# Performance work log

Measured on AMD Instinct MI355X. Metric: run time of the kernel, lower is better.

Reference implementation:

```python
import jax, jax.numpy as jnp
import numpy as np

N_NODES = 100000
N_EDGES = 1600000
N_GRAPHS = 1000
D_IN = 128
HID = 128
OUT = 6


def setup_inputs() -> dict:
    key = jax.random.key(0)
    ks = jax.random.split(key, 12)
    s = 1.0 / np.sqrt(HID)
    x = jax.random.normal(ks[0], (N_NODES, D_IN), dtype=jnp.float32)
    ei = jax.random.randint(ks[1], (2, N_EDGES), 0, N_NODES, dtype=jnp.int64)
    batch = jnp.sort(jax.random.randint(ks[2], (N_NODES,), 0, N_GRAPHS, dtype=jnp.int64))
    return {
        "x": x,
        "ei": ei,
        "batch": batch,
        "W1a": jax.random.normal(ks[3], (D_IN, HID), dtype=jnp.float32) * s,
        "b1a": jnp.zeros((HID,), jnp.float32),
        "W1b": jax.random.normal(ks[4], (HID, HID), dtype=jnp.float32) * s,
        "b1b": jnp.zeros((HID,), jnp.float32),
        "W2a": jax.random.normal(ks[5], (HID, HID), dtype=jnp.float32) * s,
        "b2a": jnp.zeros((HID,), jnp.float32),
        "W2b": jax.random.normal(ks[6], (HID, HID), dtype=jnp.float32) * s,
        "b2b": jnp.zeros((HID,), jnp.float32),
        "Wlin": jax.random.normal(ks[7], (HID, OUT), dtype=jnp.float32) * s,
        "blin": jnp.zeros((OUT,), jnp.float32),
    }


def _gin_conv(x, src, dst, Wa, ba, Wb, bb):
    # PyG GINConv (eps=0): mlp(x_i + sum_{j->i} x_j)
    agg = jax.ops.segment_sum(x[src], dst, num_segments=N_NODES)
    h = agg + x
    h = jnp.maximum(h @ Wa + ba, 0.0)
    return h @ Wb + bb


def reference(x, ei, batch, W1a, b1a, W1b, b1b, W2a, b2a, W2b, b2b, Wlin, blin):
    src, dst = ei[0], ei[1]
    h = jnp.maximum(_gin_conv(x, src, dst, W1a, b1a, W1b, b1b), 0.0)
    # dropout is identity in eval mode
    h = _gin_conv(h, src, dst, W2a, b2a, W2b, b2b)
    # global mean pool per graph
    sums = jax.ops.segment_sum(h, batch, num_segments=N_GRAPHS)
    cnts = jax.ops.segment_sum(jnp.ones((h.shape[0], 1), h.dtype), batch, num_segments=N_GRAPHS)
    pooled = sums / jnp.maximum(cnts, 1.0)
    return pooled @ Wlin + blin
```

## Files before the change

kernel.cpp:

```cpp
#include <hip/hip_runtime.h>

#define N_NODES 100000
#define N_EDGES 1600000
#define N_GRAPHS 1000
#define HID 128
#define OUTD 6

#define BUCK_LOG 7
#define BUCK_W (1 << BUCK_LOG)
#define NBUCK ((N_NODES + BUCK_W - 1) >> BUCK_LOG)
#define BCAP 4096
#define FILL_BLOCKS 256
#define FILL_CHUNK ((N_EDGES + FILL_BLOCKS - 1) / FILL_BLOCKS)

#define CVT_BLOCKS 6250
#define GST_BLOCKS 391
#define PACK_BLOCKS 32
#define PREP_BLOCKS (CVT_BLOCKS + GST_BLOCKS + PACK_BLOCKS + FILL_BLOCKS)

typedef _Float16 h2 __attribute__((ext_vector_type(2)));
typedef _Float16 half8 __attribute__((ext_vector_type(8)));
typedef float f32x4 __attribute__((ext_vector_type(4)));

__global__ __launch_bounds__(256) void k_prep(const float* __restrict__ x,
                                              const int* __restrict__ batch,
                                              const int* __restrict__ srcv,
                                              const int* __restrict__ dstv,
                                              const float* __restrict__ W1a,
                                              const float* __restrict__ W1b,
                                              const float* __restrict__ W2a,
                                              const float* __restrict__ W2b,
                                              _Float16* __restrict__ X16,
                                              int* __restrict__ gstart,
                                              _Float16* __restrict__ P,
                                              int* __restrict__ bcur0,
                                              int* __restrict__ packed) {
    __shared__ int h[NBUCK];
    __shared__ int lcur[NBUCK];
    int b = blockIdx.x, t = threadIdx.x;
    if (b < CVT_BLOCKS) {
        size_t i = ((size_t)b * 256 + t) * 8;
        float4 v0 = *(const float4*)(x + i);
        float4 v1 = *(const float4*)(x + i + 4);
        half8 o;
        o[0] = (_Float16)v0.x; o[1] = (_Float16)v0.y; o[2] = (_Float16)v0.z; o[3] = (_Float16)v0.w;
        o[4] = (_Float16)v1.x; o[5] = (_Float16)v1.y; o[6] = (_Float16)v1.z; o[7] = (_Float16)v1.w;
        *(half8*)(X16 + i) = o;
    } else if (b < CVT_BLOCKS + GST_BLOCKS) {
        int n = (b - CVT_BLOCKS) * 256 + t;
        if (n < N_NODES) {
            int bb = batch[n];
            int prev = (n == 0) ? -1 : batch[n - 1];
            for (int g = prev + 1; g <= bb; ++g) gstart[g] = n;
            if (n == N_NODES - 1)
                for (int g = bb + 1; g <= N_GRAPHS; ++g) gstart[g] = N_NODES;
        }
    } else if (b < CVT_BLOCKS + GST_BLOCKS + PACK_BLOCKS) {
        int gid = (b - CVT_BLOCKS - GST_BLOCKS) * 256 + t;
        int mat = gid >> 11;
        int r = gid & 2047;
        int ctks = r >> 6;
        int lane = r & 63;
        int col = (ctks >> 2) * 16 + (lane & 15);
        int k0 = (ctks & 3) * 32 + (lane >> 4) * 8;
        const float* W = (mat == 0) ? W1a : (mat == 1) ? W1b : (mat == 2) ? W2a : W2b;
        _Float16* dp = P + mat * 16384 + r * 8;
#pragma unroll
        for (int j = 0; j < 8; ++j) dp[j] = (_Float16)W[(k0 + j) * HID + col];
    } else {
        int bb = b - (CVT_BLOCKS + GST_BLOCKS + PACK_BLOCKS);
        int e0 = bb * FILL_CHUNK;
        int e1 = min(e0 + FILL_CHUNK, N_EDGES);
        for (int i = t; i < NBUCK; i += 256) h[i] = 0;
        __syncthreads();
        for (int e = e0 + t; e < e1; e += 256) atomicAdd(&h[dstv[e] >> BUCK_LOG], 1);
        __syncthreads();
        for (int i = t; i < NBUCK; i += 256) {
            int c = h[i];
            lcur[i] = c ? atomicAdd(&bcur0[i], c) : 0;
        }
        __syncthreads();
        for (int e = e0 + t; e < e1; e += 256) {
            int d = dstv[e];
            int bk = d >> BUCK_LOG;
            int pos = atomicAdd(&lcur[bk], 1);
            if (pos < BCAP) packed[bk * BCAP + pos] = ((d & (BUCK_W - 1)) << 20) | srcv[e];
        }
    }
}

__global__ __launch_bounds__(256) void k_csrfine(const int* __restrict__ packed,
                                                 const int* __restrict__ bcur0,
                                                 int* __restrict__ offsets,
                                                 int* __restrict__ csr_src) {
    __shared__ int hist[BUCK_W];
    __shared__ int scan[BUCK_W];
    __shared__ int cur[BUCK_W];
    __shared__ int red[4];
    int b = blockIdx.x;
    int base = b << BUCK_LOG;
    int t = threadIdx.x;
    int partial = 0;
    for (int j = t; j < b; j += 256) partial += bcur0[j];
#pragma unroll
    for (int d = 32; d > 0; d >>= 1) partial += __shfl_down(partial, d, 64);
    if ((t & 63) == 0) red[t >> 6] = partial;
    __syncthreads();
    int s = red[0] + red[1] + red[2] + red[3];
    int cnt = bcur0[b];
    const int* pb = packed + b * BCAP;

    if (t < BUCK_W) hist[t] = 0;
    __syncthreads();
    for (int i = t; i < cnt; i += 256) atomicAdd(&hist[pb[i] >> 20], 1);
    __syncthreads();
    if (t < BUCK_W) scan[t] = hist[t];
    __syncthreads();
    for (int d = 1; d < BUCK_W; d <<= 1) {
        int a = 0;
        if (t >= d && t < BUCK_W) a = scan[t - d];
        __syncthreads();
        if (t < BUCK_W) scan[t] += a;
        __syncthreads();
    }
    if (t < BUCK_W) {
        int node = base + t;
        if (node < N_NODES) {
            int excl = scan[t] - hist[t];
            offsets[node] = s + excl;
            cur[t] = excl;
        }
    }
    if (b == 0 && t == 0) offsets[N_NODES] = N_EDGES;
    __syncthreads();
    for (int i = t; i < cnt; i += 256) {
        int v = pb[i];
        int ln = v >> 20;
        int pos = atomicAdd(&cur[ln], 1);
        csr_src[s + pos] = v & 0xFFFFF;
    }
}

__global__ __launch_bounds__(256) void k_gather16(const _Float16* __restrict__ x,
                                                  const int* __restrict__ csr,
                                                  const int* __restrict__ offs,
                                                  _Float16* __restrict__ out) {
    int node = __builtin_amdgcn_readfirstlane(blockIdx.x * 4 + (threadIdx.x >> 6));
    int lane = threadIdx.x & 63;
    const h2* xp = (const h2*)x;
    int s = offs[node], e = offs[node + 1];
    h2 a0 = xp[(size_t)node * 64 + lane];
    h2 z; z[0] = (_Float16)0; z[1] = (_Float16)0;
    h2 a1 = z, a2 = z, a3 = z, a4 = z, a5 = z, a6 = z, a7 = z;
    for (int base = s; base < e; base += 64) {
        int cnt = e - base;
        if (cnt > 64) cnt = 64;
        int myidx = 0;
        if (base + lane < e) myidx = csr[base + lane];
        int j = 0;
        for (; j + 8 <= cnt; j += 8) {
            int s0 = __builtin_amdgcn_readlane(myidx, j);
            int s1 = __builtin_amdgcn_readlane(myidx, j + 1);
            int s2 = __builtin_amdgcn_readlane(myidx, j + 2);
            int s3 = __builtin_amdgcn_readlane(myidx, j + 3);
            int s4 = __builtin_amdgcn_readlane(myidx, j + 4);
            int s5 = __builtin_amdgcn_readlane(myidx, j + 5);
            int s6 = __builtin_amdgcn_readlane(myidx, j + 6);
            int s7 = __builtin_amdgcn_readlane(myidx, j + 7);
            a0 += xp[(size_t)s0 * 64 + lane];
            a1 += xp[(size_t)s1 * 64 + lane];
            a2 += xp[(size_t)s2 * 64 + lane];
            a3 += xp[(size_t)s3 * 64 + lane];
            a4 += xp[(size_t)s4 * 64 + lane];
            a5 += xp[(size_t)s5 * 64 + lane];
            a6 += xp[(size_t)s6 * 64 + lane];
            a7 += xp[(size_t)s7 * 64 + lane];
        }
        for (; j + 2 <= cnt; j += 2) {
            int s0 = __builtin_amdgcn_readlane(myidx, j);
            int s1 = __builtin_amdgcn_readlane(myidx, j + 1);
            a0 += xp[(size_t)s0 * 64 + lane];
            a1 += xp[(size_t)s1 * 64 + lane];
        }
        for (; j < cnt; ++j) {
            int sc = __builtin_amdgcn_readlane(myidx, j);
            a0 += xp[(size_t)sc * 64 + lane];
        }
    }
    h2 r = ((a0 + a1) + (a2 + a3)) + ((a4 + a5) + (a6 + a7));
    ((h2*)out)[(size_t)node * 64 + lane] = r;
}

static __device__ __forceinline__ unsigned long long pack4(float v0, float v1,
                                                           float v2, float v3) {
    union { h2 h[2]; unsigned long long u; } u;
    h2 p0, p1;
    p0[0] = (_Float16)v0; p0[1] = (_Float16)v1;
    p1[0] = (_Float16)v2; p1[1] = (_Float16)v3;
    u.h[0] = p0; u.h[1] = p1;
    return u.u;
}

template <int RELU_OUT>
__global__ __launch_bounds__(256, 2) void k_mlp16(const _Float16* __restrict__ in,
                                                  const _Float16* __restrict__ Wap,
                                                  const float* __restrict__ ba,
                                                  const _Float16* __restrict__ Wbp,
                                                  const float* __restrict__ bb,
                                                  _Float16* __restrict__ out) {
    __shared__ uint4 WaS4[2048];
    __shared__ uint4 WbS4[2048];
    __shared__ unsigned long long hS[4][512];
    int t = threadIdx.x;
    int wave = t >> 6, lane = t & 63;
    int l = lane & 15, w = lane >> 4;
    int row0 = blockIdx.x * 256 + wave * 64;

    const uint4* wa4 = (const uint4*)Wap;
    const uint4* wb4 = (const uint4*)Wbp;
#pragma unroll
    for (int i = 0; i < 8; ++i) WaS4[t + i * 256] = wa4[t + i * 256];
#pragma unroll
    for (int i = 0; i < 8; ++i) WbS4[t + i * 256] = wb4[t + i * 256];
    __syncthreads();
    const half8* waf = (const half8*)WaS4;
    const half8* wbf = (const half8*)WbS4;
    unsigned long long* h64 = hS[wave];
    int swz = ((l & 3) << 2) ^ (((l >> 2) & 1) << 1);

    float4 baR[8], bbR[8];
#pragma unroll
    for (int ct = 0; ct < 8; ++ct) {
        baR[ct] = *(const float4*)(ba + ct * 16 + w * 4);
        bbR[ct] = *(const float4*)(bb + ct * 16 + w * 4);
    }

#pragma unroll
    for (int tile = 0; tile < 4; ++tile) {
        int row = row0 + tile * 16 + l;
        bool rok = row < N_NODES;
        const _Float16* rp = in + (size_t)row * HID + w * 8;
        half8 xf[4];
#pragma unroll
        for (int ks = 0; ks < 4; ++ks) {
            half8 v = {0, 0, 0, 0, 0, 0, 0, 0};
            if (rok) v = *(const half8*)(rp + ks * 32);
            xf[ks] = v;
        }
#pragma unroll
        for (int ct = 0; ct < 8; ++ct) {
            f32x4 c = {0.f, 0.f, 0.f, 0.f};
#pragma unroll
            for (int ks = 0; ks < 4; ++ks)
                c = __builtin_amdgcn_mfma_f32_16x16x32_f16(waf[(ct * 4 + ks) * 64 + lane],
                                                           xf[ks], c, 0, 0, 0);
            float4 b4 = baR[ct];
            h64[l * 32 + ((ct * 4 + w) ^ swz)] =
                pack4(fmaxf(c[0] + b4.x, 0.f), fmaxf(c[1] + b4.y, 0.f),
                      fmaxf(c[2] + b4.z, 0.f), fmaxf(c[3] + b4.w, 0.f));
        }
        half8 hf[4];
#pragma unroll
        for (int ks = 0; ks < 4; ++ks) {
            int slot = (ks * 8 + w * 2) ^ swz;
            hf[ks] = *(const half8*)&h64[l * 32 + slot];
        }
#pragma unroll
        for (int ct = 0; ct < 8; ++ct) {
            f32x4 c = {0.f, 0.f, 0.f, 0.f};
#pragma unroll
            for (int ks = 0; ks < 4; ++ks)
                c = __builtin_amdgcn_mfma_f32_16x16x32_f16(wbf[(ct * 4 + ks) * 64 + lane],
                                                           hf[ks], c, 0, 0, 0);
            float4 b4 = bbR[ct];
            float v0 = c[0] + b4.x, v1 = c[1] + b4.y, v2 = c[2] + b4.z, v3 = c[3] + b4.w;
            if (RELU_OUT) {
                v0 = fmaxf(v0, 0.f); v1 = fmaxf(v1, 0.f);
                v2 = fmaxf(v2, 0.f); v3 = fmaxf(v3, 0.f);
            }
            if (rok)
                *(unsigned long long*)(out + (size_t)row * HID + ct * 16 + w * 4) =
                    pack4(v0, v1, v2, v3);
        }
    }
}

__global__ __launch_bounds__(256) void k_pool_head(const _Float16* __restrict__ h,
                                                   const int* __restrict__ gstart,
                                                   const float* __restrict__ Wlin,
                                                   const float* __restrict__ blin,
                                                   float* __restrict__ out) {
    __shared__ float sums[4][HID];
    int g = blockIdx.x;
    int t = threadIdx.x;
    int wave = t >> 6, lane = t & 63;
    int s = gstart[g], e = gstart[g + 1];
    float ax = 0.f, ay = 0.f;
    const h2* hp = (const h2*)h;
    int r = s + wave;
    for (; r + 12 < e; r += 16) {
        h2 v0 = hp[(size_t)r * 64 + lane];
        h2 v1 = hp[(size_t)(r + 4) * 64 + lane];
        h2 v2 = hp[(size_t)(r + 8) * 64 + lane];
        h2 v3 = hp[(size_t)(r + 12) * 64 + lane];
        ax += (float)v0[0] + (float)v1[0] + (float)v2[0] + (float)v3[0];
        ay += (float)v0[1] + (float)v1[1] + (float)v2[1] + (float)v3[1];
    }
    for (; r < e; r += 4) {
        h2 v = hp[(size_t)r * 64 + lane];
        ax += (float)v[0];
        ay += (float)v[1];
    }
    sums[wave][2 * lane] = ax;
    sums[wave][2 * lane + 1] = ay;
    __syncthreads();
    if (wave != 0) return;
    float c = fmaxf((float)(e - s), 1.0f);
    float px = (sums[0][2 * lane] + sums[1][2 * lane] + sums[2][2 * lane] + sums[3][2 * lane]) / c;
    float py = (sums[0][2 * lane + 1] + sums[1][2 * lane + 1] + sums[2][2 * lane + 1] +
                sums[3][2 * lane + 1]) / c;
#pragma unroll
    for (int o = 0; o < OUTD; ++o) {
        float v = px * Wlin[(2 * lane) * OUTD + o] + py * Wlin[(2 * lane + 1) * OUTD + o];
#pragma unroll
        for (int d = 32; d > 0; d >>= 1) v += __shfl_down(v, d, 64);
        if (lane == 0) out[g * OUTD + o] = v + blin[o];
    }
}

extern "C" void kernel_launch(void* const* d_in, const int* in_sizes, int n_in,
                              void* d_out, int out_size, void* d_ws, size_t ws_size,
                              hipStream_t stream) {
    const float* x    = (const float*)d_in[0];
    const int*   ei   = (const int*)d_in[1];
    const int*   batch= (const int*)d_in[2];
    const float* W1a  = (const float*)d_in[3];
    const float* b1a  = (const float*)d_in[4];
    const float* W1b  = (const float*)d_in[5];
    const float* b1b  = (const float*)d_in[6];
    const float* W2a  = (const float*)d_in[7];
    const float* b2a  = (const float*)d_in[8];
    const float* W2b  = (const float*)d_in[9];
    const float* b2b  = (const float*)d_in[10];
    const float* Wlin = (const float*)d_in[11];
    const float* blin = (const float*)d_in[12];
    const int* src = ei;
    const int* dst = ei + N_EDGES;
    float* out = (float*)d_out;

    char* ws = (char*)d_ws;
    size_t off = 0;
    auto alloc = [&](size_t bytes) -> void* {
        void* p = ws + off;
        off += (bytes + 255) & ~(size_t)255;
        return p;
    };
    _Float16* X16 = (_Float16*)alloc(2ull * N_NODES * HID);
    _Float16* M   = (_Float16*)alloc(2ull * N_NODES * HID + 65536);
    _Float16* H1  = (_Float16*)alloc(2ull * N_NODES * HID + 65536);
    int*   csr_src = (int*)alloc(sizeof(int) * (size_t)N_EDGES);
    int*   offsets = (int*)alloc(sizeof(int) * (N_NODES + 1));
    int*   gstart  = (int*)alloc(sizeof(int) * (N_GRAPHS + 1));
    int*   bcur0   = (int*)alloc(sizeof(int) * NBUCK);
    _Float16* Wpack = (_Float16*)alloc(2ull * 4 * 16384);
    int* packed = (int*)H1;
    _Float16* M2 = M;
    _Float16* H2 = X16;
    (void)ws_size; (void)in_sizes; (void)n_in; (void)out_size;

    hipMemsetAsync(bcur0, 0, sizeof(int) * NBUCK, stream);

    k_prep<<<PREP_BLOCKS, 256, 0, stream>>>(x, batch, src, dst, W1a, W1b, W2a, W2b,
                                            X16, gstart, Wpack, bcur0, packed);
    k_csrfine<<<NBUCK, 256, 0, stream>>>(packed, bcur0, offsets, csr_src);

    k_gather16<<<N_NODES / 4, 256, 0, stream>>>(X16, csr_src, offsets, M);
    k_mlp16<1><<<(N_NODES + 255) / 256, 256, 0, stream>>>(M, Wpack + 0 * 16384, b1a,
                                                          Wpack + 1 * 16384, b1b, H1);
    k_gather16<<<N_NODES / 4, 256, 0, stream>>>(H1, csr_src, offsets, M2);
    k_mlp16<0><<<(N_NODES + 255) / 256, 256, 0, stream>>>(M2, Wpack + 2 * 16384, b2a,
                                                          Wpack + 3 * 16384, b2b, H2);

    k_pool_head<<<N_GRAPHS, 256, 0, stream>>>(H2, gstart, Wlin, blin, out);
}
```

Before: 334.1 us.

## Front-load edge bucketing blocks, double fill blocks, vectorize edge loads

Moves the edge-bucketing fill blocks to the front of the prep grid so the long-latency atomic work starts first instead of trailing the conversion blocks. It also doubles the fill block count with smaller chunks, and reads dst/src indices as int4 with a scalar tail loop. This aims to shorten the critical tail of the prep kernel. In exchange it issues more global atomics on bucket cursors and changes the order of edges within each bucket.

```diff
diff --git a/kernel.cpp b/kernel.cpp
--- a/kernel.cpp
+++ b/kernel.cpp
@@ -10,8 +10,8 @@
 #define BUCK_W (1 << BUCK_LOG)
 #define NBUCK ((N_NODES + BUCK_W - 1) >> BUCK_LOG)
 #define BCAP 4096
-#define FILL_BLOCKS 256
-#define FILL_CHUNK ((N_EDGES + FILL_BLOCKS - 1) / FILL_BLOCKS)
+#define FILL_BLOCKS 512
+#define FILL_CHUNK 3128
 
 #define CVT_BLOCKS 6250
 #define GST_BLOCKS 391
@@ -38,16 +38,56 @@
     __shared__ int h[NBUCK];
     __shared__ int lcur[NBUCK];
     int b = blockIdx.x, t = threadIdx.x;
-    if (b < CVT_BLOCKS) {
-        size_t i = ((size_t)b * 256 + t) * 8;
+    if (b < FILL_BLOCKS) {
+        int e0 = b * FILL_CHUNK;
+        int e1 = min(e0 + FILL_CHUNK, N_EDGES);
+        for (int i = t; i < NBUCK; i += 256) h[i] = 0;
+        __syncthreads();
+        int ev = e0 + ((e1 - e0) & ~3);
+        for (int e = e0 + t * 4; e < ev; e += 1024) {
+            int4 d4 = *(const int4*)(dstv + e);
+            atomicAdd(&h[d4.x >> BUCK_LOG], 1);
+            atomicAdd(&h[d4.y >> BUCK_LOG], 1);
+            atomicAdd(&h[d4.z >> BUCK_LOG], 1);
+            atomicAdd(&h[d4.w >> BUCK_LOG], 1);
+        }
+        for (int e = ev + t; e < e1; e += 256) atomicAdd(&h[dstv[e] >> BUCK_LOG], 1);
+        __syncthreads();
+        for (int i = t; i < NBUCK; i += 256) {
+            int c = h[i];
+            lcur[i] = c ? atomicAdd(&bcur0[i], c) : 0;
+        }
+        __syncthreads();
+        for (int e = e0 + t * 4; e < ev; e += 1024) {
+            int4 d4 = *(const int4*)(dstv + e);
+            int4 s4 = *(const int4*)(srcv + e);
+            int b0 = d4.x >> BUCK_LOG, b1 = d4.y >> BUCK_LOG;
+            int b2 = d4.z >> BUCK_LOG, b3 = d4.w >> BUCK_LOG;
+            int p0 = atomicAdd(&lcur[b0], 1);
+            int p1 = atomicAdd(&lcur[b1], 1);
+            int p2 = atomicAdd(&lcur[b2], 1);
+            int p3 = atomicAdd(&lcur[b3], 1);
+            if (p0 < BCAP) packed[b0 * BCAP + p0] = ((d4.x & (BUCK_W - 1)) << 20) | s4.x;
+            if (p1 < BCAP) packed[b1 * BCAP + p1] = ((d4.y & (BUCK_W - 1)) << 20) | s4.y;
+            if (p2 < BCAP) packed[b2 * BCAP + p2] = ((d4.z & (BUCK_W - 1)) << 20) | s4.z;
+            if (p3 < BCAP) packed[b3 * BCAP + p3] = ((d4.w & (BUCK_W - 1)) << 20) | s4.w;
+        }
+        for (int e = ev + t; e < e1; e += 256) {
+            int d = dstv[e];
+            int bk = d >> BUCK_LOG;
+            int pos = atomicAdd(&lcur[bk], 1);
+            if (pos < BCAP) packed[bk * BCAP + pos] = ((d & (BUCK_W - 1)) << 20) | srcv[e];
+        }
+    } else if (b < FILL_BLOCKS + CVT_BLOCKS) {
+        size_t i = ((size_t)(b - FILL_BLOCKS) * 256 + t) * 8;
         float4 v0 = *(const float4*)(x + i);
         float4 v1 = *(const float4*)(x + i + 4);
         half8 o;
         o[0] = (_Float16)v0.x; o[1] = (_Float16)v0.y; o[2] = (_Float16)v0.z; o[3] = (_Float16)v0.w;
         o[4] = (_Float16)v1.x; o[5] = (_Float16)v1.y; o[6] = (_Float16)v1.z; o[7] = (_Float16)v1.w;
         *(half8*)(X16 + i) = o;
-    } else if (b < CVT_BLOCKS + GST_BLOCKS) {
-        int n = (b - CVT_BLOCKS) * 256 + t;
+    } else if (b < FILL_BLOCKS + CVT_BLOCKS + GST_BLOCKS) {
+        int n = (b - FILL_BLOCKS - CVT_BLOCKS) * 256 + t;
         if (n < N_NODES) {
             int bb = batch[n];
             int prev = (n == 0) ? -1 : batch[n - 1];
@@ -55,8 +95,8 @@
             if (n == N_NODES - 1)
                 for (int g = bb + 1; g <= N_GRAPHS; ++g) gstart[g] = N_NODES;
         }
-    } else if (b < CVT_BLOCKS + GST_BLOCKS + PACK_BLOCKS) {
-        int gid = (b - CVT_BLOCKS - GST_BLOCKS) * 256 + t;
+    } else {
+        int gid = (b - FILL_BLOCKS - CVT_BLOCKS - GST_BLOCKS) * 256 + t;
         int mat = gid >> 11;
         int r = gid & 2047;
         int ctks = r >> 6;
@@ -67,25 +107,6 @@
         _Float16* dp = P + mat * 16384 + r * 8;
 #pragma unroll
         for (int j = 0; j < 8; ++j) dp[j] = (_Float16)W[(k0 + j) * HID + col];
-    } else {
-        int bb = b - (CVT_BLOCKS + GST_BLOCKS + PACK_BLOCKS);
-        int e0 = bb * FILL_CHUNK;
-        int e1 = min(e0 + FILL_CHUNK, N_EDGES);
-        for (int i = t; i < NBUCK; i += 256) h[i] = 0;
-        __syncthreads();
-        for (int e = e0 + t; e < e1; e += 256) atomicAdd(&h[dstv[e] >> BUCK_LOG], 1);
-        __syncthreads();
-        for (int i = t; i < NBUCK; i += 256) {
-            int c = h[i];
-            lcur[i] = c ? atomicAdd(&bcur0[i], c) : 0;
-        }
-        __syncthreads();
-        for (int e = e0 + t; e < e1; e += 256) {
-            int d = dstv[e];
-            int bk = d >> BUCK_LOG;
-            int pos = atomicAdd(&lcur[bk], 1);
-            if (pos < BCAP) packed[bk * BCAP + pos] = ((d & (BUCK_W - 1)) << 20) | srcv[e];
-        }
     }
 }
 
```

Result: faster. 310.3 us (-7.1%).
